# Kernel tuning notes

Measured on AMD Instinct MI355X. Metric: run time of the kernel, lower is better.

## Reference

```python
import jax, jax.numpy as jnp
import numpy as np

B, S, D_MODEL, H, OUT = 32, 64, 256, 256, 10
N_POS = 64  # n_max_seq + 1


def _coordinate_map():
    i = jnp.arange(N_POS, dtype=jnp.float32)
    r = jnp.sqrt(jnp.float32(N_POS))
    c0 = (i / r - 2.0) / 2.0
    c1 = (jnp.mod(i, r) - 2.0) / 2.0
    coord = jnp.stack([c0, c1], axis=-1)            # [N_POS, 2]
    return jnp.broadcast_to(coord[None], (B, N_POS, 2))


def setup_inputs() -> dict:
    key = jax.random.key(0)
    ks = jax.random.split(key, 13)
    d_in = (D_MODEL + 2) * 3
    w = lambda k, i, o: jax.random.normal(k, (i, o), jnp.float32) * 0.02
    b = lambda k, o: jax.random.normal(k, (o,), jnp.float32) * 0.02
    return {
        'sentences': jax.random.normal(ks[0], (B, S, D_MODEL), jnp.float32),
        'coord': _coordinate_map(),
        'g_w1': w(ks[1], d_in, H), 'g_b1': b(ks[2], H),
        'g_w2': w(ks[3], H, H),    'g_b2': b(ks[4], H),
        'g_w3': w(ks[5], H, H),    'g_b3': b(ks[6], H),
        'f_w1': w(ks[7], H, H),    'f_b1': b(ks[8], H),
        'f_w2': w(ks[9], H, H),    'f_b2': b(ks[10], H),
        'f_w3': w(ks[11], H, OUT), 'f_b3': b(ks[12], OUT),
    }


def reference(sentences, coord, g_w1, g_b1, g_w2, g_b2, g_w3, g_b3,
              f_w1, f_b1, f_w2, f_b2, f_w3, f_b3):
    b, s, d = sentences.shape
    x = jnp.concatenate([sentences, coord[:b, :s, :]], axis=-1)   # [B,S,D+2]
    oi = jnp.broadcast_to(x[:, None, :, :], (b, s, s, d + 2))     # object_i[b,i,j]=x[b,j]
    oj = jnp.broadcast_to(x[:, :, None, :], (b, s, s, d + 2))     # object_j[b,i,j]=x[b,i]
    pairs = jnp.concatenate([oi, oj, oi * oj], axis=-1)           # [B,S,S,3*(D+2)]
    h = jax.nn.relu(jnp.einsum('bijk,kh->bijh', pairs, g_w1) + g_b1)
    h = jax.nn.relu(h @ g_w2 + g_b2)
    h = jax.nn.relu(h @ g_w3 + g_b3)
    rel = h.reshape(b, s * s, -1).sum(axis=1)                     # [B,H]
    y = jax.nn.relu(rel @ f_w1 + f_b1)
    y = jax.nn.relu(y @ f_w2 + f_b2)                              # Dropout: eval mode (identity)
    return y @ f_w3 + f_b3                                        # [B,OUT]
```

## Files before the change

kernel.cpp:

```cpp
#include <hip/hip_runtime.h>
#include <hip/hip_bf16.h>


typedef __attribute__((ext_vector_type(4))) float f32x4;
typedef __attribute__((ext_vector_type(16))) float f32x16;
typedef __attribute__((ext_vector_type(8))) short frag8;

__device__ __forceinline__ float bf2f(short s) {
  return __uint_as_float(((unsigned)(unsigned short)s) << 16);
}
__device__ __forceinline__ short f2bf(float f) {
  unsigned u = __float_as_uint(f);
  return (short)((u + 0x7fffu + ((u >> 16) & 1u)) >> 16);
}

#define KX 288

__global__ __launch_bounds__(256)
void prep(const float* __restrict__ sent, const float* __restrict__ coord,
          const float* __restrict__ g_w1, const float* __restrict__ g_w2,
          const float* __restrict__ g_w3,
          short* __restrict__ xb, short* __restrict__ Wab, short* __restrict__ Wc,
          short* __restrict__ W2t, short* __restrict__ W3t, float* __restrict__ rel) {
  __shared__ short tile[64 * 66];
  const int blk = blockIdx.x, t = threadIdx.x;

  if (blk < 288) {
    long idx0 = ((long)blk * 256 + t) * 8;
#pragma unroll
    for (int e = 0; e < 8; e++) {
      long idx = idx0 + e;
      int row = (int)(idx / KX), k = (int)(idx - (long)row * KX);
      float v = 0.f;
      if (k < 256)      v = sent[(size_t)row * 256 + k];
      else if (k < 258) v = coord[row * 2 + (k - 256)];
      xb[idx] = f2bf(v);
    }
    return;
  }

  const int nc = t & 63, r4 = t >> 6;
  if (blk < 328) {
    int tt = blk - 288, kt = tt >> 3, nt = tt & 7;
    int k0 = kt * 64, n0 = nt * 64;
    for (int p = 0; p < 16; p++) {
      int kl = p * 4 + r4, k = k0 + kl, n = n0 + nc;
      float v = 0.f;
      if (k < 258) {
        int row = (n < 256) ? k : 258 + k;
        int col = (n < 256) ? n : n - 256;
        v = g_w1[(size_t)row * 256 + col];
      }
      tile[kl * 66 + nc] = f2bf(v);
    }
    __syncthreads();
    for (int p = 0; p < 16; p++) {
      int nl = p * 4 + r4;
      if (k0 + nc < KX) Wab[(size_t)(n0 + nl) * KX + k0 + nc] = tile[nc * 66 + nl];
    }
    return;
  }
  if (blk < 348) {
    int tt = blk - 328, kt = tt >> 2, nt = tt & 3;
    int k0 = kt * 64, n0 = nt * 64;
    for (int p = 0; p < 16; p++) {
      int kl = p * 4 + r4, k = k0 + kl;
      float v = (k < 258) ? g_w1[(size_t)(516 + k) * 256 + n0 + nc] : 0.f;
      tile[kl * 66 + nc] = f2bf(v);
    }
    __syncthreads();
    for (int p = 0; p < 16; p++) {
      int nl = p * 4 + r4;
      if (k0 + nc < KX) Wc[(size_t)(n0 + nl) * KX + k0 + nc] = tile[nc * 66 + nl];
    }
    return;
  }
  if (blk < 380) {
    int tt = blk - 348;
    const float* W = (tt < 16) ? g_w2 : g_w3;
    short* Wt = (tt < 16) ? W2t : W3t;
    tt &= 15;
    int k0 = (tt >> 2) * 64, n0 = (tt & 3) * 64;
    for (int p = 0; p < 16; p++) {
      int kl = p * 4 + r4;
      tile[kl * 66 + nc] = f2bf(W[(size_t)(k0 + kl) * 256 + n0 + nc]);
    }
    __syncthreads();
    for (int p = 0; p < 16; p++) {
      int nl = p * 4 + r4;
      Wt[(size_t)(n0 + nl) * 256 + k0 + nc] = tile[nc * 66 + nl];
    }
    return;
  }
  {
    int bb = blk - 380;
    ((f32x4*)rel)[bb * 256 + t] = (f32x4){0.f, 0.f, 0.f, 0.f};
  }
}


__global__ __launch_bounds__(64)
void uv_gemm(const short* __restrict__ xb, const short* __restrict__ Wab,
             const float* __restrict__ g_b1, float* __restrict__ uv) {
  const int m0 = blockIdx.x * 64;
  const int n0 = blockIdx.y * 64;
  const int lane = threadIdx.x;
  const int q = lane >> 4, l16 = lane & 15;

  f32x4 acc[4][4];
#pragma unroll
  for (int mt = 0; mt < 4; mt++)
#pragma unroll
    for (int nt = 0; nt < 4; nt++) acc[mt][nt] = (f32x4){0.f, 0.f, 0.f, 0.f};

  for (int k0 = 0; k0 < KX; k0 += 32) {
    frag8 a[4], bb[4];
#pragma unroll
    for (int mt = 0; mt < 4; mt++)
      a[mt] = *(const frag8*)(xb + (size_t)(m0 + mt * 16 + l16) * KX + k0 + q * 8);
#pragma unroll
    for (int nt = 0; nt < 4; nt++)
      bb[nt] = *(const frag8*)(Wab + (size_t)(n0 + nt * 16 + l16) * KX + k0 + q * 8);
#pragma unroll
    for (int mt = 0; mt < 4; mt++)
#pragma unroll
      for (int nt = 0; nt < 4; nt++)
        acc[mt][nt] = __builtin_amdgcn_mfma_f32_16x16x32_bf16(a[mt], bb[nt], acc[mt][nt], 0, 0, 0);
  }
#pragma unroll
  for (int nt = 0; nt < 4; nt++) {
    int col = n0 + nt * 16 + l16;
    float bias = (col >= 256) ? g_b1[col - 256] : 0.f;
#pragma unroll
    for (int mt = 0; mt < 4; mt++) {
      int m = m0 + mt * 16 + q * 4;
#pragma unroll
      for (int r = 0; r < 4; r++)
        uv[(size_t)(m + r) * 512 + col] = acc[mt][nt][r] + bias;
    }
  }
}


#define ASH 152
#define LDS_SHORTS 32768

__global__ __launch_bounds__(256, 2)
void relnet_main(const short* __restrict__ xb, const short* __restrict__ Wc,
                 const short* __restrict__ W2t, const short* __restrict__ W3t,
                 const float* __restrict__ uv, const float* __restrict__ g_b2,
                 const float* __restrict__ g_b3, float* __restrict__ rel) {
  __shared__ short lds[LDS_SHORTS];

  const int tid = threadIdx.x;
  const int bi = blockIdx.x;
  const int b = bi >> 5, ip = bi & 31;
  const int i0 = ip * 2;
  const int lane = tid & 63, wave = tid >> 6;
  const int l32 = lane & 31, half = lane >> 5;
  const int n0 = wave * 64;
  const int rowbase = b * 64;

  f32x16 acc[4][2];
#pragma unroll
  for (int mt = 0; mt < 4; mt++)
#pragma unroll
    for (int nt = 0; nt < 2; nt++)
#pragma unroll
      for (int r = 0; r < 16; r++) acc[mt][nt][r] = 0.f;

#pragma unroll
  for (int h = 0; h < 2; h++) {
    const int kbase = h * 144;
#pragma unroll
    for (int it = 0; it < 9; it++) {
      int idx = tid + it * 256;
      int j = idx / 18, c = idx - j * 18;
      int k = kbase + c * 8;
      int jj = j & 63, iL = j >> 6;
      frag8 aj = *(const frag8*)(xb + (size_t)(rowbase + jj) * KX + k);
      frag8 ai = *(const frag8*)(xb + (size_t)(rowbase + i0 + iL) * KX + k);
      frag8 r;
#pragma unroll
      for (int t = 0; t < 8; t++) r[t] = f2bf(bf2f(aj[t]) * bf2f(ai[t]));
      *(frag8*)(&lds[j * ASH + c * 8]) = r;
    }
    __syncthreads();

    {
      frag8 a0[4], b0[2], a1[4], b1[2];
#pragma unroll
      for (int mt = 0; mt < 4; mt++)
        a0[mt] = *(const frag8*)(&lds[(mt * 32 + l32) * ASH + half * 8]);
#pragma unroll
      for (int nt = 0; nt < 2; nt++)
        b0[nt] = *(const frag8*)(Wc + (size_t)(n0 + nt * 32 + l32) * KX + kbase + half * 8);
#pragma unroll
      for (int ks = 0; ks < 9; ks++) {
        if (ks < 8) {
          int k1 = (ks + 1) * 16 + half * 8;
#pragma unroll
          for (int mt = 0; mt < 4; mt++)
            a1[mt] = *(const frag8*)(&lds[(mt * 32 + l32) * ASH + k1]);
#pragma unroll
          for (int nt = 0; nt < 2; nt++)
            b1[nt] = *(const frag8*)(Wc + (size_t)(n0 + nt * 32 + l32) * KX + kbase + k1);
        }
#pragma unroll
        for (int mt = 0; mt < 4; mt++)
#pragma unroll
          for (int nt = 0; nt < 2; nt++)
            acc[mt][nt] = __builtin_amdgcn_mfma_f32_32x32x16_bf16(a0[mt], b0[nt], acc[mt][nt], 0, 0, 0);
#pragma unroll
        for (int mt = 0; mt < 4; mt++) a0[mt] = a1[mt];
#pragma unroll
        for (int nt = 0; nt < 2; nt++) b0[nt] = b1[nt];
      }
    }
    __syncthreads();
  }

  {
    const float* ub = uv + (size_t)rowbase * 512;
    const float* v0p = uv + (size_t)(rowbase + i0) * 512 + 256;
    const float* v1p = uv + (size_t)(rowbase + i0 + 1) * 512 + 256;
#pragma unroll
    for (int nt = 0; nt < 2; nt++) {
      int col = n0 + nt * 32 + l32;
      int cb = (n0 + nt * 32) >> 3;
      float vv0 = v0p[col], vv1 = v1p[col];
#pragma unroll
      for (int mt = 0; mt < 4; mt++) {
        float vv = (mt < 2) ? vv0 : vv1;
#pragma unroll
        for (int r = 0; r < 16; r++) {
          int rowbits = (r & 3) + 8 * (r >> 2) + 4 * half;
          int jm = (mt & 1) * 32 + rowbits;
          int m = mt * 32 + rowbits;
          float val = acc[mt][nt][r] + ub[(size_t)jm * 512 + col] + vv;
          int sw = (r & 3) + 4 * half;
          lds[m * 256 + (((cb + (l32 >> 3)) ^ sw) << 3) + (l32 & 7)] = f2bf(fmaxf(val, 0.f));
        }
#pragma unroll
        for (int r = 0; r < 16; r++) acc[mt][nt][r] = 0.f;
      }
    }
  }
  __syncthreads();

  {
    const int swr = l32 & 7;
    frag8 a0[4], b0[2], a1[4], b1[2];
#pragma unroll
    for (int mt = 0; mt < 4; mt++)
      a0[mt] = *(const frag8*)(&lds[(mt * 32 + l32) * 256 + ((half ^ swr) << 3)]);
#pragma unroll
    for (int nt = 0; nt < 2; nt++)
      b0[nt] = *(const frag8*)(W2t + (size_t)(n0 + nt * 32 + l32) * 256 + half * 8);
#pragma unroll
    for (int ks = 0; ks < 16; ks++) {
      if (ks < 15) {
        int c1 = ((2 * (ks + 1) + half) ^ swr) << 3;
        int k1 = (ks + 1) * 16 + half * 8;
#pragma unroll
        for (int mt = 0; mt < 4; mt++)
          a1[mt] = *(const frag8*)(&lds[(mt * 32 + l32) * 256 + c1]);
#pragma unroll
        for (int nt = 0; nt < 2; nt++)
          b1[nt] = *(const frag8*)(W2t + (size_t)(n0 + nt * 32 + l32) * 256 + k1);
      }
#pragma unroll
      for (int mt = 0; mt < 4; mt++)
#pragma unroll
        for (int nt = 0; nt < 2; nt++)
          acc[mt][nt] = __builtin_amdgcn_mfma_f32_32x32x16_bf16(a0[mt], b0[nt], acc[mt][nt], 0, 0, 0);
#pragma unroll
      for (int mt = 0; mt < 4; mt++) a0[mt] = a1[mt];
#pragma unroll
      for (int nt = 0; nt < 2; nt++) b0[nt] = b1[nt];
    }
  }
  __syncthreads();
#pragma unroll
  for (int nt = 0; nt < 2; nt++) {
    int col = n0 + nt * 32 + l32;
    int cb = (n0 + nt * 32) >> 3;
    float b2 = g_b2[col];
#pragma unroll
    for (int mt = 0; mt < 4; mt++) {
#pragma unroll
      for (int r = 0; r < 16; r++) {
        int rowbits = (r & 3) + 8 * (r >> 2) + 4 * half;
        int m = mt * 32 + rowbits;
        int sw = (r & 3) + 4 * half;
        lds[m * 256 + (((cb + (l32 >> 3)) ^ sw) << 3) + (l32 & 7)] =
            f2bf(fmaxf(acc[mt][nt][r] + b2, 0.f));
      }
#pragma unroll
      for (int r = 0; r < 16; r++) acc[mt][nt][r] = 0.f;
    }
  }
  __syncthreads();

  {
    const int swr = l32 & 7;
    frag8 a0[4], b0[2], a1[4], b1[2];
#pragma unroll
    for (int mt = 0; mt < 4; mt++)
      a0[mt] = *(const frag8*)(&lds[(mt * 32 + l32) * 256 + ((half ^ swr) << 3)]);
#pragma unroll
    for (int nt = 0; nt < 2; nt++)
      b0[nt] = *(const frag8*)(W3t + (size_t)(n0 + nt * 32 + l32) * 256 + half * 8);
#pragma unroll
    for (int ks = 0; ks < 16; ks++) {
      if (ks < 15) {
        int c1 = ((2 * (ks + 1) + half) ^ swr) << 3;
        int k1 = (ks + 1) * 16 + half * 8;
#pragma unroll
        for (int mt = 0; mt < 4; mt++)
          a1[mt] = *(const frag8*)(&lds[(mt * 32 + l32) * 256 + c1]);
#pragma unroll
        for (int nt = 0; nt < 2; nt++)
          b1[nt] = *(const frag8*)(W3t + (size_t)(n0 + nt * 32 + l32) * 256 + k1);
      }
#pragma unroll
      for (int mt = 0; mt < 4; mt++)
#pragma unroll
        for (int nt = 0; nt < 2; nt++)
          acc[mt][nt] = __builtin_amdgcn_mfma_f32_32x32x16_bf16(a0[mt], b0[nt], acc[mt][nt], 0, 0, 0);
#pragma unroll
      for (int mt = 0; mt < 4; mt++) a0[mt] = a1[mt];
#pragma unroll
      for (int nt = 0; nt < 2; nt++) b0[nt] = b1[nt];
    }
  }
#pragma unroll
  for (int nt = 0; nt < 2; nt++) {
    int col = n0 + nt * 32 + l32;
    float b3 = g_b3[col];
    float s = 0.f;
#pragma unroll
    for (int mt = 0; mt < 4; mt++)
#pragma unroll
      for (int r = 0; r < 16; r++)
        s += fmaxf(acc[mt][nt][r] + b3, 0.f);
    s += __shfl_xor(s, 32, 64);
    if (half == 0) atomicAdd(&rel[b * 256 + col], s);
  }
}

__global__ __launch_bounds__(256)
void fnet(const float* __restrict__ rel, const float* __restrict__ f_w1,
          const float* __restrict__ f_b1, const float* __restrict__ f_w2,
          const float* __restrict__ f_b2, const float* __restrict__ f_w3,
          const float* __restrict__ f_b3, float* __restrict__ out) {
  int b = blockIdx.x, t = threadIdx.x;
  __shared__ float y0[256], y1[256], y2[256];
  y0[t] = rel[b * 256 + t];
  __syncthreads();
  float s = f_b1[t];
#pragma unroll 8
  for (int k = 0; k < 256; k++) s += y0[k] * f_w1[k * 256 + t];
  y1[t] = fmaxf(s, 0.f);
  __syncthreads();
  s = f_b2[t];
#pragma unroll 8
  for (int k = 0; k < 256; k++) s += y1[k] * f_w2[k * 256 + t];
  y2[t] = fmaxf(s, 0.f);
  __syncthreads();
  if (t < 10) {
    float s2 = f_b3[t];
#pragma unroll 8
    for (int k = 0; k < 256; k++) s2 += y2[k] * f_w3[k * 10 + t];
    out[b * 10 + t] = s2;
  }
}

extern "C" void kernel_launch(void* const* d_in, const int* in_sizes, int n_in,
                              void* d_out, int out_size, void* d_ws, size_t ws_size,
                              hipStream_t stream) {
  const float* sent  = (const float*)d_in[0];
  const float* coord = (const float*)d_in[1];
  const float* g_w1  = (const float*)d_in[2];
  const float* g_b1  = (const float*)d_in[3];
  const float* g_w2  = (const float*)d_in[4];
  const float* g_b2  = (const float*)d_in[5];
  const float* g_w3  = (const float*)d_in[6];
  const float* g_b3  = (const float*)d_in[7];
  const float* f_w1  = (const float*)d_in[8];
  const float* f_b1  = (const float*)d_in[9];
  const float* f_w2  = (const float*)d_in[10];
  const float* f_b2  = (const float*)d_in[11];
  const float* f_w3  = (const float*)d_in[12];
  const float* f_b3  = (const float*)d_in[13];
  float* out = (float*)d_out;

  char* ws = (char*)d_ws;
  size_t off = 0;
  auto alloc = [&](size_t bytes) {
    char* p = ws + off;
    off += (bytes + 255) & ~(size_t)255;
    return p;
  };
  short* xb  = (short*)alloc((size_t)2048 * KX * 2);
  short* Wab = (short*)alloc((size_t)512 * KX * 2);
  short* Wc  = (short*)alloc((size_t)256 * KX * 2);
  short* W2t = (short*)alloc((size_t)256 * 256 * 2);
  short* W3t = (short*)alloc((size_t)256 * 256 * 2);
  float* uv  = (float*)alloc((size_t)2048 * 512 * 4);
  float* rel = (float*)alloc((size_t)32 * 256 * 4);

  prep<<<388, 256, 0, stream>>>(sent, coord, g_w1, g_w2, g_w3, xb, Wab, Wc, W2t, W3t, rel);
  uv_gemm<<<dim3(32, 8), 64, 0, stream>>>(xb, Wab, g_b1, uv);
  relnet_main<<<1024, 256, 0, stream>>>(xb, Wc, W2t, W3t, uv, g_b2, g_b3, rel);
  fnet<<<32, 256, 0, stream>>>(rel, f_w1, f_b1, f_w2, f_b2, f_w3, f_b3, out);
}
```

Before: 184.6 us.

## Compute pairwise product operands in registers instead of staging through LDS

The first GEMM stage no longer builds the xj*xi product tile in shared memory with two barriers per half. Each lane now loads its xj and xi fragments directly from global memory, multiplies them in packed bf16 pairs, and feeds the result straight into MFMA over all 18 k-steps. The epilogues also use a packed bf16 conversion helper, which uses the hardware cvt_pk builtin when it exists. This removes LDS writes, reads and barriers, but adds redundant global loads and per-lane multiply work across the four waves.

```diff
diff --git a/kernel.cpp b/kernel.cpp
--- a/kernel.cpp
+++ b/kernel.cpp
@@ -5,6 +5,7 @@
 typedef __attribute__((ext_vector_type(4))) float f32x4;
 typedef __attribute__((ext_vector_type(16))) float f32x16;
 typedef __attribute__((ext_vector_type(8))) short frag8;
+typedef __attribute__((ext_vector_type(4))) unsigned u32x4;
 
 __device__ __forceinline__ float bf2f(short s) {
   return __uint_as_float(((unsigned)(unsigned short)s) << 16);
@@ -12,6 +13,32 @@
 __device__ __forceinline__ short f2bf(float f) {
   unsigned u = __float_as_uint(f);
   return (short)((u + 0x7fffu + ((u >> 16) & 1u)) >> 16);
+}
+
+__device__ __forceinline__ unsigned pk_bf16(float lo, float hi) {
+#if __has_builtin(__builtin_amdgcn_cvt_pk_bf16_f32)
+  return __builtin_bit_cast(unsigned, __builtin_amdgcn_cvt_pk_bf16_f32(lo, hi));
+#else
+  unsigned ul = __float_as_uint(lo), uh = __float_as_uint(hi);
+  ul = (ul + 0x7fffu + ((ul >> 16) & 1u)) >> 16;
+  uh = (uh + 0x7fffu + ((uh >> 16) & 1u)) & 0xffff0000u;
+  return ul | uh;
+#endif
+}
+
+__device__ __forceinline__ unsigned pk_mul_bf16(unsigned a, unsigned b) {
+  float al = __uint_as_float(a << 16);
+  float ah = __uint_as_float(a & 0xffff0000u);
+  float bl = __uint_as_float(b << 16);
+  float bh = __uint_as_float(b & 0xffff0000u);
+  return pk_bf16(al * bl, ah * bh);
+}
+
+__device__ __forceinline__ frag8 pk_mul4(u32x4 a, u32x4 b) {
+  u32x4 r;
+#pragma unroll
+  for (int t = 0; t < 4; t++) r[t] = pk_mul_bf16(a[t], b[t]);
+  return __builtin_bit_cast(frag8, r);
 }
 
 #define KX 288
@@ -142,7 +169,6 @@
 }
 
 
-#define ASH 152
 #define LDS_SHORTS 32768
 
 __global__ __launch_bounds__(256, 2)
@@ -169,55 +195,49 @@
 #pragma unroll
       for (int r = 0; r < 16; r++) acc[mt][nt][r] = 0.f;
 
-#pragma unroll
-  for (int h = 0; h < 2; h++) {
-    const int kbase = h * 144;
-#pragma unroll
-    for (int it = 0; it < 9; it++) {
-      int idx = tid + it * 256;
-      int j = idx / 18, c = idx - j * 18;
-      int k = kbase + c * 8;
-      int jj = j & 63, iL = j >> 6;
-      frag8 aj = *(const frag8*)(xb + (size_t)(rowbase + jj) * KX + k);
-      frag8 ai = *(const frag8*)(xb + (size_t)(rowbase + i0 + iL) * KX + k);
-      frag8 r;
-#pragma unroll
-      for (int t = 0; t < 8; t++) r[t] = f2bf(bf2f(aj[t]) * bf2f(ai[t]));
-      *(frag8*)(&lds[j * ASH + c * 8]) = r;
-    }
-    __syncthreads();
-
+  {
+    const short* xjl = xb + (size_t)(rowbase + l32) * KX;
+    const short* xjh = xb + (size_t)(rowbase + 32 + l32) * KX;
+    const short* xi0p = xb + (size_t)(rowbase + i0) * KX;
+    const short* xi1p = xb + (size_t)(rowbase + i0 + 1) * KX;
+    const short* wc0 = Wc + (size_t)(n0 + l32) * KX;
+    const short* wc1 = Wc + (size_t)(n0 + 32 + l32) * KX;
+
+    u32x4 jl0, jh0, ia0, ib0, jl1, jh1, ia1, ib1;
+    frag8 b0[2], b1[2];
     {
-      frag8 a0[4], b0[2], a1[4], b1[2];
+      int k = half * 8;
+      jl0 = *(const u32x4*)(xjl + k);
+      jh0 = *(const u32x4*)(xjh + k);
+      ia0 = *(const u32x4*)(xi0p + k);
+      ib0 = *(const u32x4*)(xi1p + k);
+      b0[0] = *(const frag8*)(wc0 + k);
+      b0[1] = *(const frag8*)(wc1 + k);
+    }
+#pragma unroll
+    for (int ks = 0; ks < 18; ks++) {
+      if (ks < 17) {
+        int k = (ks + 1) * 16 + half * 8;
+        jl1 = *(const u32x4*)(xjl + k);
+        jh1 = *(const u32x4*)(xjh + k);
+        ia1 = *(const u32x4*)(xi0p + k);
+        ib1 = *(const u32x4*)(xi1p + k);
+        b1[0] = *(const frag8*)(wc0 + k);
+        b1[1] = *(const frag8*)(wc1 + k);
+      }
+      frag8 a[4];
+      a[0] = pk_mul4(jl0, ia0);
+      a[1] = pk_mul4(jh0, ia0);
+      a[2] = pk_mul4(jl0, ib0);
+      a[3] = pk_mul4(jh0, ib0);
 #pragma unroll
       for (int mt = 0; mt < 4; mt++)
-        a0[mt] = *(const frag8*)(&lds[(mt * 32 + l32) * ASH + half * 8]);
-#pragma unroll
-      for (int nt = 0; nt < 2; nt++)
-        b0[nt] = *(const frag8*)(Wc + (size_t)(n0 + nt * 32 + l32) * KX + kbase + half * 8);
-#pragma unroll
-      for (int ks = 0; ks < 9; ks++) {
-        if (ks < 8) {
-          int k1 = (ks + 1) * 16 + half * 8;
-#pragma unroll
-          for (int mt = 0; mt < 4; mt++)
-            a1[mt] = *(const frag8*)(&lds[(mt * 32 + l32) * ASH + k1]);
-#pragma unroll
-          for (int nt = 0; nt < 2; nt++)
-            b1[nt] = *(const frag8*)(Wc + (size_t)(n0 + nt * 32 + l32) * KX + kbase + k1);
-        }
-#pragma unroll
-        for (int mt = 0; mt < 4; mt++)
-#pragma unroll
-          for (int nt = 0; nt < 2; nt++)
-            acc[mt][nt] = __builtin_amdgcn_mfma_f32_32x32x16_bf16(a0[mt], b0[nt], acc[mt][nt], 0, 0, 0);
-#pragma unroll
-        for (int mt = 0; mt < 4; mt++) a0[mt] = a1[mt];
-#pragma unroll
-        for (int nt = 0; nt < 2; nt++) b0[nt] = b1[nt];
-      }
-    }
-    __syncthreads();
+#pragma unroll
+        for (int nt = 0; nt < 2; nt++)
+          acc[mt][nt] = __builtin_amdgcn_mfma_f32_32x32x16_bf16(a[mt], b0[nt], acc[mt][nt], 0, 0, 0);
+      jl0 = jl1; jh0 = jh1; ia0 = ia1; ib0 = ib1;
+      b0[0] = b1[0]; b0[1] = b1[1];
+    }
   }
 
   {
@@ -233,13 +253,16 @@
       for (int mt = 0; mt < 4; mt++) {
         float vv = (mt < 2) ? vv0 : vv1;
 #pragma unroll
-        for (int r = 0; r < 16; r++) {
-          int rowbits = (r & 3) + 8 * (r >> 2) + 4 * half;
-          int jm = (mt & 1) * 32 + rowbits;
-          int m = mt * 32 + rowbits;
-          float val = acc[mt][nt][r] + ub[(size_t)jm * 512 + col] + vv;
-          int sw = (r & 3) + 4 * half;
-          lds[m * 256 + (((cb + (l32 >> 3)) ^ sw) << 3) + (l32 & 7)] = f2bf(fmaxf(val, 0.f));
+        for (int r = 0; r < 16; r += 2) {
+          int rb0 = (r & 3) + 8 * (r >> 2) + 4 * half;
+          int jm0 = (mt & 1) * 32 + rb0;
+          float x0 = fmaxf(acc[mt][nt][r]     + ub[(size_t)jm0 * 512 + col] + vv, 0.f);
+          float x1 = fmaxf(acc[mt][nt][r + 1] + ub[(size_t)(jm0 + 1) * 512 + col] + vv, 0.f);
+          unsigned pk = pk_bf16(x0, x1);
+          int m0r = mt * 32 + rb0;
+          int sw0 = (r & 3) + 4 * half;
+          lds[m0r * 256 + (((cb + (l32 >> 3)) ^ sw0) << 3) + (l32 & 7)] = (short)(pk & 0xffffu);
+          lds[(m0r + 1) * 256 + (((cb + (l32 >> 3)) ^ (sw0 + 1)) << 3) + (l32 & 7)] = (short)(pk >> 16);
         }
 #pragma unroll
         for (int r = 0; r < 16; r++) acc[mt][nt][r] = 0.f;
@@ -289,12 +312,15 @@
 #pragma unroll
     for (int mt = 0; mt < 4; mt++) {
 #pragma unroll
-      for (int r = 0; r < 16; r++) {
-        int rowbits = (r & 3) + 8 * (r >> 2) + 4 * half;
-        int m = mt * 32 + rowbits;
-        int sw = (r & 3) + 4 * half;
-        lds[m * 256 + (((cb + (l32 >> 3)) ^ sw) << 3) + (l32 & 7)] =
-            f2bf(fmaxf(acc[mt][nt][r] + b2, 0.f));
+      for (int r = 0; r < 16; r += 2) {
+        int rb0 = (r & 3) + 8 * (r >> 2) + 4 * half;
+        float x0 = fmaxf(acc[mt][nt][r] + b2, 0.f);
+        float x1 = fmaxf(acc[mt][nt][r + 1] + b2, 0.f);
+        unsigned pk = pk_bf16(x0, x1);
+        int m0r = mt * 32 + rb0;
+        int sw0 = (r & 3) + 4 * half;
+        lds[m0r * 256 + (((cb + (l32 >> 3)) ^ sw0) << 3) + (l32 & 7)] = (short)(pk & 0xffffu);
+        lds[(m0r + 1) * 256 + (((cb + (l32 >> 3)) ^ (sw0 + 1)) << 3) + (l32 & 7)] = (short)(pk >> 16);
       }
 #pragma unroll
       for (int r = 0; r < 16; r++) acc[mt][nt][r] = 0.f;
```

New measurement: 195.2 us. 5.8% more time.
